# Kernel optimization log

Hardware: AMD Instinct MI355X
Metric: run time of the kernel (lower is better)

The kernel has to match this reference:

```python
import jax, jax.numpy as jnp
import numpy as np

N_GRAPHS = 512


def setup_inputs() -> dict:
    key = jax.random.key(0)
    ks = jax.random.split(key, 9)
    N, E, V, NE, D, C = 100000, 500000, 50000, 1000000, 300, 20
    nodes_batch = jax.random.randint(ks[0], (N,), 0, V)
    edges_batch = jax.random.randint(ks[1], (E,), 0, NE)
    src = jax.random.randint(ks[2], (E,), 0, N)
    dst = jax.random.randint(ks[3], (E,), 0, N)
    graph_ids = jnp.sort(jax.random.randint(ks[4], (N,), 0, N_GRAPHS))
    node_embed = jax.random.normal(ks[5], (V, D), dtype=jnp.float32)
    edge_embed = jax.random.uniform(ks[6], (NE, 1), dtype=jnp.float32)
    fc_w = jax.random.normal(ks[7], (D, C), dtype=jnp.float32) * 0.05
    fc_b = jnp.zeros((C,), dtype=jnp.float32)
    return {"nodes_batch": nodes_batch, "edges_batch": edges_batch, "src": src,
            "dst": dst, "graph_ids": graph_ids, "node_embed": node_embed,
            "edge_embed": edge_embed, "fc_w": fc_w, "fc_b": fc_b}


def reference(nodes_batch, edges_batch, src, dst, graph_ids, node_embed, edge_embed, fc_w, fc_b):
    N = nodes_batch.shape[0]
    h = node_embed[nodes_batch]                      # [N, D] node features
    w = edge_embed[edges_batch]                      # [E, 1] scalar edge weights
    msg = h[src] * w                                 # [E, D] src_mul_edge
    # DGL mean reduce over incoming edges; nodes with no in-edges get 0.
    summed = jax.ops.segment_sum(msg, dst, num_segments=N)
    cnt = jax.ops.segment_sum(jnp.ones((msg.shape[0],), msg.dtype), dst, num_segments=N)
    h_new = summed / jnp.maximum(cnt, 1.0)[:, None]  # [N, D]
    g = jax.ops.segment_sum(h_new, graph_ids, num_segments=N_GRAPHS)  # sum_nodes readout
    out = jax.nn.relu(g) @ fc_w + fc_b               # dropout is identity at eval
    return out
```

## Files before the change

kernel.cpp:

```cpp
#include <hip/hip_runtime.h>
#include <hip/hip_bf16.h>

#define NG 512
#define D_DIM 300
#define C_DIM 20
#define NSLICE 8
#define NBINS (NSLICE * NG)
#define GSTRIDE 304
#define CAP 320
#define VPAD 16

static __device__ inline ushort f2bf(float f) {
    union { float f; unsigned u; } x; x.f = f;
    unsigned r = x.u + 0x7FFF + ((x.u >> 16) & 1);
    return (ushort)(r >> 16);
}

__global__ __launch_bounds__(256) void fb_count(const int* __restrict__ dst,
                                                int* __restrict__ cnt, int E) {
    int e = blockIdx.x * 256 + threadIdx.x;
    if (e < E) atomicAdd(&cnt[dst[e]], 1);
}

__global__ __launch_bounds__(256) void convert_b(const float* __restrict__ B,
                                                 ushort* __restrict__ B16, int K) {
    int total = K * 38;
    int gs = gridDim.x * 256;
    for (int i0 = blockIdx.x * 256 + threadIdx.x; i0 < total; i0 += 2 * gs) {
        int i1 = i0 + gs;
        bool ok1 = i1 < total;
        int r0 = i0 / 38, k0 = i0 - r0 * 38, d00 = k0 * 8;
        int r1 = 0, k1, d01 = 0;
        if (ok1) { r1 = i1 / 38; k1 = i1 - r1 * 38; d01 = k1 * 8; }
        const float* p0 = B + (size_t)r0 * D_DIM + d00;
        const float* p1 = ok1 ? (B + (size_t)r1 * D_DIM + d01) : p0;
        float4 a0 = *(const float4*)p0;
        float4 b0 = (d00 + 8 <= D_DIM) ? *(const float4*)(p0 + 4) : make_float4(0.f, 0.f, 0.f, 0.f);
        float4 a1 = *(const float4*)p1;
        float4 b1 = (d01 + 8 <= D_DIM) ? *(const float4*)(p1 + 4) : make_float4(0.f, 0.f, 0.f, 0.f);
        uint4 q0;
        q0.x = (unsigned)f2bf(a0.x) | ((unsigned)f2bf(a0.y) << 16);
        q0.y = (unsigned)f2bf(a0.z) | ((unsigned)f2bf(a0.w) << 16);
        q0.z = (unsigned)f2bf(b0.x) | ((unsigned)f2bf(b0.y) << 16);
        q0.w = (unsigned)f2bf(b0.z) | ((unsigned)f2bf(b0.w) << 16);
        *(uint4*)(B16 + (size_t)r0 * GSTRIDE + d00) = q0;
        if (ok1) {
            uint4 q1;
            q1.x = (unsigned)f2bf(a1.x) | ((unsigned)f2bf(a1.y) << 16);
            q1.y = (unsigned)f2bf(a1.z) | ((unsigned)f2bf(a1.w) << 16);
            q1.z = (unsigned)f2bf(b1.x) | ((unsigned)f2bf(b1.y) << 16);
            q1.w = (unsigned)f2bf(b1.z) | ((unsigned)f2bf(b1.w) << 16);
            *(uint4*)(B16 + (size_t)r1 * GSTRIDE + d01) = q1;
        }
    }
}

__global__ __launch_bounds__(256) void scatter_direct(const int* __restrict__ src,
                                                      const int* __restrict__ dst,
                                                      const int* __restrict__ eb,
                                                      const int* __restrict__ nodes_batch,
                                                      const int* __restrict__ graph_ids,
                                                      const float* __restrict__ edge_embed,
                                                      const int* __restrict__ cnt,
                                                      int* __restrict__ vdeg,
                                                      int2* __restrict__ bucket,
                                                      int E, int KS) {
    int e = blockIdx.x * 256 + threadIdx.x;
    if (e >= E) return;
    int d = dst[e];
    int v = nodes_batch[src[e]];
    int g = graph_ids[d];
    int bin = (v / KS) * NG + g;
    float s = edge_embed[eb[e]] / (float)max(cnt[d], 1);
    int pos = atomicAdd(&vdeg[bin * VPAD], 1);
    if (pos < CAP)
        bucket[(size_t)bin * CAP + pos] = make_int2(v, __float_as_int(s));
}

static __device__ inline void acc8(uint4 q, float s, float* a) {
    a[0] += s * __uint_as_float(q.x << 16);
    a[1] += s * __uint_as_float(q.x & 0xFFFF0000u);
    a[2] += s * __uint_as_float(q.y << 16);
    a[3] += s * __uint_as_float(q.y & 0xFFFF0000u);
    a[4] += s * __uint_as_float(q.z << 16);
    a[5] += s * __uint_as_float(q.z & 0xFFFF0000u);
    a[6] += s * __uint_as_float(q.w << 16);
    a[7] += s * __uint_as_float(q.w & 0xFFFF0000u);
}

__global__ __launch_bounds__(256, 4) void accum_wave(const int2* __restrict__ bucket,
                                                     const int* __restrict__ vdeg,
                                                     const ushort* __restrict__ B16,
                                                     float* __restrict__ gslice) {
    int t = threadIdx.x;
    int wv = t >> 6, lane = t & 63;
    if (lane >= 38) return;
    int slice = blockIdx.x & 7;
    int g = ((blockIdx.x >> 3) << 1) + (wv >> 1);
    int h = wv & 1;
    int bin = slice * NG + g;
    int deg = min(vdeg[bin * VPAD], CAP);
    int base = bin * CAP;
    int mid = deg >> 1;
    int beg = base + (h ? mid : 0);
    int end = base + (h ? deg : mid);
    const ushort* Bl = B16 + (lane << 3);

    float a[8] = {0.f, 0.f, 0.f, 0.f, 0.f, 0.f, 0.f, 0.f};
    int j = beg;
    for (; j + 8 <= end; j += 8) {
        int2 p0 = bucket[j + 0], p1 = bucket[j + 1], p2 = bucket[j + 2], p3 = bucket[j + 3];
        int2 p4 = bucket[j + 4], p5 = bucket[j + 5], p6 = bucket[j + 6], p7 = bucket[j + 7];
        uint4 q0 = *(const uint4*)(Bl + (size_t)p0.x * GSTRIDE);
        uint4 q1 = *(const uint4*)(Bl + (size_t)p1.x * GSTRIDE);
        uint4 q2 = *(const uint4*)(Bl + (size_t)p2.x * GSTRIDE);
        uint4 q3 = *(const uint4*)(Bl + (size_t)p3.x * GSTRIDE);
        uint4 q4 = *(const uint4*)(Bl + (size_t)p4.x * GSTRIDE);
        uint4 q5 = *(const uint4*)(Bl + (size_t)p5.x * GSTRIDE);
        uint4 q6 = *(const uint4*)(Bl + (size_t)p6.x * GSTRIDE);
        uint4 q7 = *(const uint4*)(Bl + (size_t)p7.x * GSTRIDE);
        acc8(q0, __int_as_float(p0.y), a);
        acc8(q1, __int_as_float(p1.y), a);
        acc8(q2, __int_as_float(p2.y), a);
        acc8(q3, __int_as_float(p3.y), a);
        acc8(q4, __int_as_float(p4.y), a);
        acc8(q5, __int_as_float(p5.y), a);
        acc8(q6, __int_as_float(p6.y), a);
        acc8(q7, __int_as_float(p7.y), a);
    }
    for (; j + 4 <= end; j += 4) {
        int2 p0 = bucket[j + 0], p1 = bucket[j + 1], p2 = bucket[j + 2], p3 = bucket[j + 3];
        uint4 q0 = *(const uint4*)(Bl + (size_t)p0.x * GSTRIDE);
        uint4 q1 = *(const uint4*)(Bl + (size_t)p1.x * GSTRIDE);
        uint4 q2 = *(const uint4*)(Bl + (size_t)p2.x * GSTRIDE);
        uint4 q3 = *(const uint4*)(Bl + (size_t)p3.x * GSTRIDE);
        acc8(q0, __int_as_float(p0.y), a);
        acc8(q1, __int_as_float(p1.y), a);
        acc8(q2, __int_as_float(p2.y), a);
        acc8(q3, __int_as_float(p3.y), a);
    }
    for (; j < end; ++j) {
        int2 pr = bucket[j];
        uint4 q = *(const uint4*)(Bl + (size_t)pr.x * GSTRIDE);
        acc8(q, __int_as_float(pr.y), a);
    }
    float4* outp = (float4*)(gslice + (size_t)(h * NBINS + bin) * GSTRIDE + (lane << 3));
    outp[0] = make_float4(a[0], a[1], a[2], a[3]);
    outp[1] = make_float4(a[4], a[5], a[6], a[7]);
}

__global__ __launch_bounds__(320) void fc_kernel(const float* __restrict__ gslice,
                                                 const float* __restrict__ fc_w,
                                                 const float* __restrict__ fc_b,
                                                 float* __restrict__ out) {
    __shared__ float wlds[D_DIM * C_DIM];
    __shared__ float accs[D_DIM];
    __shared__ float outs[C_DIM];
    int gid = blockIdx.x;
    int t = threadIdx.x;
    for (int i = t; i < D_DIM * C_DIM; i += 320) wlds[i] = fc_w[i];
    if (t < D_DIM) {
        float a = 0.f;
#pragma unroll
        for (int p = 0; p < 2 * NSLICE; p++)
            a += gslice[(size_t)(p * NG + gid) * GSTRIDE + t];
        accs[t] = a;
    }
    if (t < C_DIM) outs[t] = fc_b[t];
    __syncthreads();
    if (t < C_DIM * 12) {
        int c = t % C_DIM;
        int ch = t / C_DIM;
        float p = 0.f;
#pragma unroll
        for (int d = ch * 25; d < ch * 25 + 25; d++) {
            float gv = accs[d];
            gv = gv > 0.f ? gv : 0.f;
            p += gv * wlds[d * C_DIM + c];
        }
        atomicAdd(&outs[c], p);
    }
    __syncthreads();
    if (t < C_DIM) out[gid * C_DIM + t] = outs[t];
}

extern "C" void kernel_launch(void* const* d_in, const int* in_sizes, int n_in,
                              void* d_out, int out_size, void* d_ws, size_t ws_size,
                              hipStream_t stream) {
    const int* nodes_batch = (const int*)d_in[0];
    const int* edges_batch = (const int*)d_in[1];
    const int* src = (const int*)d_in[2];
    const int* dst = (const int*)d_in[3];
    const int* graph_ids = (const int*)d_in[4];
    const float* node_embed = (const float*)d_in[5];
    const float* edge_embed = (const float*)d_in[6];
    const float* fc_w = (const float*)d_in[7];
    const float* fc_b = (const float*)d_in[8];
    float* out = (float*)d_out;

    int N = in_sizes[0];
    int E = in_sizes[2];
    int K = in_sizes[5] / D_DIM;
    int KS = (K + NSLICE - 1) / NSLICE;

    char* ws = (char*)d_ws;
    size_t off = 0;
    int* cnt = (int*)(ws + off); off += (size_t)N * 4;
    off = (off + 63) & ~(size_t)63;
    int* vdeg = (int*)(ws + off); off += (size_t)NBINS * VPAD * 4;
    off = (off + 15) & ~(size_t)15;
    ushort* B16 = (ushort*)(ws + off); off += (size_t)K * GSTRIDE * 2;
    float* gslice = (float*)(ws + off); off += (size_t)2 * NBINS * GSTRIDE * 4;
    int2* bucket = (int2*)(ws + off); off += (size_t)NBINS * CAP * 8;

    if (ws_size >= off) {
        int eb_blocks = (E + 255) / 256;
        hipMemsetAsync(cnt, 0, (size_t)N * 4, stream);
        hipMemsetAsync(vdeg, 0, (size_t)NBINS * VPAD * 4, stream);
        fb_count<<<eb_blocks, 256, 0, stream>>>(dst, cnt, E);
        convert_b<<<2048, 256, 0, stream>>>(node_embed, B16, K);
        scatter_direct<<<eb_blocks, 256, 0, stream>>>(src, dst, edges_batch, nodes_batch,
                                                      graph_ids, edge_embed, cnt, vdeg,
                                                      bucket, E, KS);
        accum_wave<<<8 * (NG / 2), 256, 0, stream>>>(bucket, vdeg, B16, gslice);
        fc_kernel<<<NG, 320, 0, stream>>>(gslice, fc_w, fc_b, out);
    }
}
```

Baseline: 116.8 us.

## Fuse in-degree count into scatter and defer mean normalization to accumulation

Removes the separate in-degree counting kernel by doing the count atomics inside the scatter kernel. The normalization by in-degree moves into the accumulation kernel. The destination node index is packed into the bucket entry: 16 bits beside the vocabulary index and 1 bit stolen from the weight's mantissa LSB. The two memsets are merged into one. This saves a launch and a pass over dst, but adds a random cnt gather and a divide per edge in the hot accumulation loop. The packing assumes node and vocab indices fit in 17 and 16 bits, and it perturbs the edge weight's lowest mantissa bit.

```diff
diff --git a/kernel.cpp b/kernel.cpp
--- a/kernel.cpp
+++ b/kernel.cpp
@@ -14,12 +14,6 @@
     union { float f; unsigned u; } x; x.f = f;
     unsigned r = x.u + 0x7FFF + ((x.u >> 16) & 1);
     return (ushort)(r >> 16);
-}
-
-__global__ __launch_bounds__(256) void fb_count(const int* __restrict__ dst,
-                                                int* __restrict__ cnt, int E) {
-    int e = blockIdx.x * 256 + threadIdx.x;
-    if (e < E) atomicAdd(&cnt[dst[e]], 1);
 }
 
 __global__ __launch_bounds__(256) void convert_b(const float* __restrict__ B,
@@ -61,7 +55,7 @@
                                                       const int* __restrict__ nodes_batch,
                                                       const int* __restrict__ graph_ids,
                                                       const float* __restrict__ edge_embed,
-                                                      const int* __restrict__ cnt,
+                                                      int* __restrict__ cnt,
                                                       int* __restrict__ vdeg,
                                                       int2* __restrict__ bucket,
                                                       int E, int KS) {
@@ -70,11 +64,17 @@
     int d = dst[e];
     int v = nodes_batch[src[e]];
     int g = graph_ids[d];
+    float w = edge_embed[eb[e]];
+    atomicAdd(&cnt[d], 1);
     int bin = (v / KS) * NG + g;
-    float s = edge_embed[eb[e]] / (float)max(cnt[d], 1);
     int pos = atomicAdd(&vdeg[bin * VPAD], 1);
-    if (pos < CAP)
-        bucket[(size_t)bin * CAP + pos] = make_int2(v, __float_as_int(s));
+    if (pos < CAP) {
+        unsigned wx = __float_as_uint(w);
+        int2 entry;
+        entry.x = v | ((d & 0xFFFF) << 16);
+        entry.y = (int)((wx & ~1u) | ((unsigned)d >> 16));
+        bucket[(size_t)bin * CAP + pos] = entry;
+    }
 }
 
 static __device__ inline void acc8(uint4 q, float s, float* a) {
@@ -90,6 +90,7 @@
 
 __global__ __launch_bounds__(256, 4) void accum_wave(const int2* __restrict__ bucket,
                                                      const int* __restrict__ vdeg,
+                                                     const int* __restrict__ cnt,
                                                      const ushort* __restrict__ B16,
                                                      float* __restrict__ gslice) {
     int t = threadIdx.x;
@@ -111,38 +112,45 @@
     for (; j + 8 <= end; j += 8) {
         int2 p0 = bucket[j + 0], p1 = bucket[j + 1], p2 = bucket[j + 2], p3 = bucket[j + 3];
         int2 p4 = bucket[j + 4], p5 = bucket[j + 5], p6 = bucket[j + 6], p7 = bucket[j + 7];
-        uint4 q0 = *(const uint4*)(Bl + (size_t)p0.x * GSTRIDE);
-        uint4 q1 = *(const uint4*)(Bl + (size_t)p1.x * GSTRIDE);
-        uint4 q2 = *(const uint4*)(Bl + (size_t)p2.x * GSTRIDE);
-        uint4 q3 = *(const uint4*)(Bl + (size_t)p3.x * GSTRIDE);
-        uint4 q4 = *(const uint4*)(Bl + (size_t)p4.x * GSTRIDE);
-        uint4 q5 = *(const uint4*)(Bl + (size_t)p5.x * GSTRIDE);
-        uint4 q6 = *(const uint4*)(Bl + (size_t)p6.x * GSTRIDE);
-        uint4 q7 = *(const uint4*)(Bl + (size_t)p7.x * GSTRIDE);
-        acc8(q0, __int_as_float(p0.y), a);
-        acc8(q1, __int_as_float(p1.y), a);
-        acc8(q2, __int_as_float(p2.y), a);
-        acc8(q3, __int_as_float(p3.y), a);
-        acc8(q4, __int_as_float(p4.y), a);
-        acc8(q5, __int_as_float(p5.y), a);
-        acc8(q6, __int_as_float(p6.y), a);
-        acc8(q7, __int_as_float(p7.y), a);
-    }
-    for (; j + 4 <= end; j += 4) {
-        int2 p0 = bucket[j + 0], p1 = bucket[j + 1], p2 = bucket[j + 2], p3 = bucket[j + 3];
-        uint4 q0 = *(const uint4*)(Bl + (size_t)p0.x * GSTRIDE);
-        uint4 q1 = *(const uint4*)(Bl + (size_t)p1.x * GSTRIDE);
-        uint4 q2 = *(const uint4*)(Bl + (size_t)p2.x * GSTRIDE);
-        uint4 q3 = *(const uint4*)(Bl + (size_t)p3.x * GSTRIDE);
-        acc8(q0, __int_as_float(p0.y), a);
-        acc8(q1, __int_as_float(p1.y), a);
-        acc8(q2, __int_as_float(p2.y), a);
-        acc8(q3, __int_as_float(p3.y), a);
+        int v0 = p0.x & 0xFFFF, v1 = p1.x & 0xFFFF, v2 = p2.x & 0xFFFF, v3 = p3.x & 0xFFFF;
+        int v4 = p4.x & 0xFFFF, v5 = p5.x & 0xFFFF, v6 = p6.x & 0xFFFF, v7 = p7.x & 0xFFFF;
+        int d0 = ((unsigned)p0.x >> 16) | (((unsigned)p0.y & 1u) << 16);
+        int d1 = ((unsigned)p1.x >> 16) | (((unsigned)p1.y & 1u) << 16);
+        int d2 = ((unsigned)p2.x >> 16) | (((unsigned)p2.y & 1u) << 16);
+        int d3 = ((unsigned)p3.x >> 16) | (((unsigned)p3.y & 1u) << 16);
+        int d4 = ((unsigned)p4.x >> 16) | (((unsigned)p4.y & 1u) << 16);
+        int d5 = ((unsigned)p5.x >> 16) | (((unsigned)p5.y & 1u) << 16);
+        int d6 = ((unsigned)p6.x >> 16) | (((unsigned)p6.y & 1u) << 16);
+        int d7 = ((unsigned)p7.x >> 16) | (((unsigned)p7.y & 1u) << 16);
+        uint4 q0 = *(const uint4*)(Bl + (size_t)v0 * GSTRIDE);
+        uint4 q1 = *(const uint4*)(Bl + (size_t)v1 * GSTRIDE);
+        uint4 q2 = *(const uint4*)(Bl + (size_t)v2 * GSTRIDE);
+        uint4 q3 = *(const uint4*)(Bl + (size_t)v3 * GSTRIDE);
+        uint4 q4 = *(const uint4*)(Bl + (size_t)v4 * GSTRIDE);
+        uint4 q5 = *(const uint4*)(Bl + (size_t)v5 * GSTRIDE);
+        uint4 q6 = *(const uint4*)(Bl + (size_t)v6 * GSTRIDE);
+        uint4 q7 = *(const uint4*)(Bl + (size_t)v7 * GSTRIDE);
+        int c0 = cnt[d0], c1 = cnt[d1], c2 = cnt[d2], c3 = cnt[d3];
+        int c4 = cnt[d4], c5 = cnt[d5], c6 = cnt[d6], c7 = cnt[d7];
+        float s0 = __uint_as_float((unsigned)p0.y & ~1u) / (float)max(c0, 1);
+        float s1 = __uint_as_float((unsigned)p1.y & ~1u) / (float)max(c1, 1);
+        float s2 = __uint_as_float((unsigned)p2.y & ~1u) / (float)max(c2, 1);
+        float s3 = __uint_as_float((unsigned)p3.y & ~1u) / (float)max(c3, 1);
+        float s4 = __uint_as_float((unsigned)p4.y & ~1u) / (float)max(c4, 1);
+        float s5 = __uint_as_float((unsigned)p5.y & ~1u) / (float)max(c5, 1);
+        float s6 = __uint_as_float((unsigned)p6.y & ~1u) / (float)max(c6, 1);
+        float s7 = __uint_as_float((unsigned)p7.y & ~1u) / (float)max(c7, 1);
+        acc8(q0, s0, a); acc8(q1, s1, a); acc8(q2, s2, a); acc8(q3, s3, a);
+        acc8(q4, s4, a); acc8(q5, s5, a); acc8(q6, s6, a); acc8(q7, s7, a);
     }
     for (; j < end; ++j) {
         int2 pr = bucket[j];
-        uint4 q = *(const uint4*)(Bl + (size_t)pr.x * GSTRIDE);
-        acc8(q, __int_as_float(pr.y), a);
+        int v = pr.x & 0xFFFF;
+        int d = ((unsigned)pr.x >> 16) | (((unsigned)pr.y & 1u) << 16);
+        uint4 q = *(const uint4*)(Bl + (size_t)v * GSTRIDE);
+        int c = cnt[d];
+        float s = __uint_as_float((unsigned)pr.y & ~1u) / (float)max(c, 1);
+        acc8(q, s, a);
     }
     float4* outp = (float4*)(gslice + (size_t)(h * NBINS + bin) * GSTRIDE + (lane << 3));
     outp[0] = make_float4(a[0], a[1], a[2], a[3]);
@@ -208,6 +216,7 @@
     int* cnt = (int*)(ws + off); off += (size_t)N * 4;
     off = (off + 63) & ~(size_t)63;
     int* vdeg = (int*)(ws + off); off += (size_t)NBINS * VPAD * 4;
+    size_t zero_bytes = off;
     off = (off + 15) & ~(size_t)15;
     ushort* B16 = (ushort*)(ws + off); off += (size_t)K * GSTRIDE * 2;
     float* gslice = (float*)(ws + off); off += (size_t)2 * NBINS * GSTRIDE * 4;
@@ -215,14 +224,12 @@
 
     if (ws_size >= off) {
         int eb_blocks = (E + 255) / 256;
-        hipMemsetAsync(cnt, 0, (size_t)N * 4, stream);
-        hipMemsetAsync(vdeg, 0, (size_t)NBINS * VPAD * 4, stream);
-        fb_count<<<eb_blocks, 256, 0, stream>>>(dst, cnt, E);
+        hipMemsetAsync(ws, 0, zero_bytes, stream);
         convert_b<<<2048, 256, 0, stream>>>(node_embed, B16, K);
         scatter_direct<<<eb_blocks, 256, 0, stream>>>(src, dst, edges_batch, nodes_batch,
                                                       graph_ids, edge_embed, cnt, vdeg,
                                                       bucket, E, KS);
-        accum_wave<<<8 * (NG / 2), 256, 0, stream>>>(bucket, vdeg, B16, gslice);
+        accum_wave<<<8 * (NG / 2), 256, 0, stream>>>(bucket, vdeg, cnt, B16, gslice);
         fc_kernel<<<NG, 320, 0, stream>>>(gslice, fc_w, fc_b, out);
     }
 }
```

Measured after the change: 124.2 us. 6.3% more time.
